# Kernel optimization log

Hardware: AMD Instinct MI355X
Metric: run time of the kernel (lower is better)

The kernel has to match this reference:

```python
import jax, jax.numpy as jnp
from jax import lax
import numpy as np

L, QD, B = 16, 2048, 4096


def setup_inputs() -> dict:
    key = jax.random.key(0)
    k1, k2, k3, k4 = jax.random.split(key, 4)
    input_state = jax.random.normal(k1, (B, QD), dtype=jnp.float32)
    # rotation_angles ~ U(-0.1, 0.1) per _initialize_parameters
    rotation_angles = jax.random.uniform(k2, (L, QD, 3), dtype=jnp.float32, minval=-0.1, maxval=0.1)
    # xavier_uniform for [qd, qd] weights: bound = sqrt(6 / (qd + qd))
    bound = float(np.sqrt(6.0 / (QD + QD)))
    entanglement_weights = jax.random.uniform(k3, (L, QD, QD), dtype=jnp.float32, minval=-bound, maxval=bound)
    # orthogonal init for measurement basis via QR
    m = jax.random.normal(k4, (QD, QD), dtype=jnp.float32)
    q, r = jnp.linalg.qr(m)
    measurement_basis = (q * jnp.sign(jnp.diagonal(r))).astype(jnp.float32)
    return {
        "input_state": input_state,
        "rotation_angles": rotation_angles,
        "entanglement_weights": entanglement_weights,
        "measurement_basis": measurement_basis,
    }


def reference(input_state, rotation_angles, entanglement_weights, measurement_basis):
    # Each rotation gate reduces to an elementwise scale by cos(angle/2):
    #   x-gate: real(rot[0,0]) = cos(a/2); y-gate: cos(a/2); z-gate: real(exp(-i a/2)) = cos(a/2).
    # Fuse all three gates per layer into one per-dim scale: [L, QD]
    scales = jnp.prod(jnp.cos(rotation_angles * 0.5), axis=-1)

    def layer_step(state, layer_params):
        scale, w = layer_params  # scale: [QD], w: [QD, QD]
        return jnp.matmul(state * scale, w), None

    state, _ = lax.scan(layer_step, input_state, (scales, entanglement_weights))
    return jnp.matmul(state, measurement_basis)
```

## Files before the change

kernel.cpp:

```cpp
#include <hip/hip_runtime.h>
#include <stdint.h>

#define L_LAYERS 16
#define QD 2048
#define BATCH 4096

typedef __attribute__((ext_vector_type(8))) __bf16 bf16x8;
typedef __attribute__((ext_vector_type(4))) float f32x4;
typedef __attribute__((address_space(3))) uint32_t lds32_t;
typedef const __attribute__((address_space(1))) uint32_t glob32_t;

__device__ __forceinline__ void async_load16(const void* g, void* l) {
    __builtin_amdgcn_global_load_lds((glob32_t*)(uintptr_t)g, (lds32_t*)(uintptr_t)l,
                                     16, 0, 0);
}

__device__ __forceinline__ unsigned short f2bf(float f) {
    uint32_t u = __float_as_uint(f);
    u += 0x7FFFu + ((u >> 16) & 1u);
    return (unsigned short)(u >> 16);
}

__device__ __forceinline__ float layer_scale(const float* __restrict__ ang,
                                             int lay, int k) {
    const float* ap = ang + ((size_t)lay * QD + k) * 3;
    return __cosf(ap[0] * 0.5f) * __cosf(ap[1] * 0.5f) * __cosf(ap[2] * 0.5f);
}

__global__ void convert_in_kernel(const float* __restrict__ in,
                                  unsigned short* __restrict__ out, int n4) {
    int i = blockIdx.x * 256 + threadIdx.x;
    if (i < n4) {
        float4 v = ((const float4*)in)[i];
        ushort4 o;
        o.x = f2bf(v.x); o.y = f2bf(v.y); o.z = f2bf(v.z); o.w = f2bf(v.w);
        ((ushort4*)out)[i] = o;
    }
}

__global__ void convert_a_all(const float* __restrict__ W, const float* __restrict__ ang,
                              unsigned short* __restrict__ out) {
    const int z = blockIdx.z;
    const float* src = W + (size_t)(2 * z) * QD * QD;
    unsigned short* dst = out + (size_t)z * QD * QD;
    int i = blockIdx.x * 256 + threadIdx.x;
    float s = layer_scale(ang, 2 * z, i >> 9);
    float4 v = ((const float4*)src)[i];
    ushort4 o;
    o.x = f2bf(v.x * s); o.y = f2bf(v.y * s); o.z = f2bf(v.z * s); o.w = f2bf(v.w * s);
    ((ushort4*)dst)[i] = o;
}

__device__ __forceinline__ void conv_tile_body(const float* __restrict__ src,
                                               const float* __restrict__ ang,
                                               int lay,
                                               unsigned short* __restrict__ dst) {
    __shared__ __align__(16) unsigned short tile[64][64];
    const int t = threadIdx.x;
    const int k0 = blockIdx.y * 64, n0 = blockIdx.x * 64;
    const int r = t >> 4;
    const int c = (t & 15) * 4;
    const int g = (t & 7) << 3;
#pragma unroll
    for (int rr = 0; rr < 64; rr += 16) {
        int k = k0 + r + rr;
        float s = (lay >= 0) ? layer_scale(ang, lay, k) : 1.0f;
        float4 v = *(const float4*)(src + (size_t)k * QD + n0 + c);
        int col = (r + rr) ^ g;
        tile[c + 0][col] = f2bf(v.x * s);
        tile[c + 1][col] = f2bf(v.y * s);
        tile[c + 2][col] = f2bf(v.z * s);
        tile[c + 3][col] = f2bf(v.w * s);
    }
    __syncthreads();
    const int wr = t >> 3;
    const int wc = (t & 7) * 8;
#pragma unroll
    for (int rr = 0; rr < 64; rr += 32) {
        int row = wr + rr;
        int pc = wc ^ (((row >> 2) & 7) << 3);
        *(float4*)(dst + (size_t)(n0 + row) * QD + k0 + wc) =
            *(const float4*)(&tile[row][pc]);
    }
}

__global__ void convert_b_all(const float* __restrict__ W, const float* __restrict__ Mb,
                              const float* __restrict__ ang, unsigned short* __restrict__ out) {
    const int z = blockIdx.z;
    const float* src = (z < 8) ? (W + (size_t)(2 * z + 1) * QD * QD) : Mb;
    const int lay = (z < 8) ? (2 * z + 1) : -1;
    unsigned short* dst = out + (size_t)z * QD * QD;
    conv_tile_body(src, ang, lay, dst);
}

struct GemmBatch {
    const unsigned short* a[8];
    const unsigned short* b[8];
    void* c[8];
};

template <int OUT_BF16, int TM>
__global__ __launch_bounds__(256, TM == 128 ? 2 : 4)
void gemm_kernel(GemmBatch args) {
    constexpr int NI = TM / 32;
    __shared__ __align__(16) unsigned short ldsA[TM * 64];
    __shared__ __align__(16) unsigned short ldsB[128 * 64];
    const unsigned short* __restrict__ A  = args.a[blockIdx.z];
    const unsigned short* __restrict__ Bt = args.b[blockIdx.z];
    void* __restrict__ Cout = args.c[blockIdx.z];

    const int t = threadIdx.x;
    const int n0 = blockIdx.x * 128;
    const int m0 = blockIdx.y * TM;
    const int lane = t & 63;
    const int wave = t >> 6;
    const int wm = (wave & 1) * (TM / 2);
    const int wn = (wave >> 1) * 64;
    const int fr = lane & 15;
    const int quad = lane >> 4;

    f32x4 acc[NI][4] = {};

    const int sr = t >> 2;
    const int scol = (t & 3) * 8;
    const unsigned short* ga = A + (size_t)(m0 + sr) * QD + scol;
    const unsigned short* gb = Bt + (size_t)(n0 + sr) * QD + scol;
    unsigned short* la = ldsA + t * 8;
    unsigned short* lb = ldsB + t * 8;

    for (int k0 = 0; k0 < QD; k0 += 64) {
        __syncthreads();
        if constexpr (TM == 128) {
            async_load16(ga, la);
            async_load16(ga + 64 * QD, la + 2048);
            async_load16(ga + 32, la + 4096);
            async_load16(ga + 32 + 64 * QD, la + 6144);
        } else {
            async_load16(ga, la);
            async_load16(ga + 32, la + 2048);
        }
        async_load16(gb, lb);
        async_load16(gb + 64 * QD, lb + 2048);
        async_load16(gb + 32, lb + 4096);
        async_load16(gb + 32 + 64 * QD, lb + 6144);
        ga += 64;
        gb += 64;
        __syncthreads();

#pragma unroll
        for (int kk = 0; kk < 2; kk++) {
            const unsigned short* pa = ldsA + kk * (TM * 32);
            const unsigned short* pb = ldsB + kk * 4096;
            bf16x8 af[NI], bfr[4];
#pragma unroll
            for (int i = 0; i < NI; i++)
                af[i] = *(const bf16x8*)(pa + (wm + i * 16 + fr) * 32 + quad * 8);
#pragma unroll
            for (int j = 0; j < 4; j++)
                bfr[j] = *(const bf16x8*)(pb + (wn + j * 16 + fr) * 32 + quad * 8);
#pragma unroll
            for (int i = 0; i < NI; i++)
#pragma unroll
                for (int j = 0; j < 4; j++)
                    acc[i][j] = __builtin_amdgcn_mfma_f32_16x16x32_bf16(af[i], bfr[j],
                                                                        acc[i][j], 0, 0, 0);
        }
    }

#pragma unroll
    for (int i = 0; i < NI; i++) {
        const int gr = m0 + wm + i * 16 + quad * 4;
#pragma unroll
        for (int j = 0; j < 4; j++) {
            const int gc = n0 + wn + j * 16 + fr;
#pragma unroll
            for (int r = 0; r < 4; r++) {
                float v = acc[i][j][r];
                if (OUT_BF16)
                    ((unsigned short*)Cout)[(size_t)(gr + r) * QD + gc] = f2bf(v);
                else
                    ((float*)Cout)[(size_t)(gr + r) * QD + gc] = v;
            }
        }
    }
}

__device__ __forceinline__ void stage_half(const unsigned short* __restrict__ G,
                                           int row0, int k0,
                                           unsigned char* dst, int t) {
    const int r = t >> 3;
    const int c = 8 * ((t & 7) ^ (r & 7));
    const unsigned short* g = G + (size_t)(row0 + r) * QD + k0 + c;
    async_load16(g, dst + t * 16);
    async_load16(g + 64 * QD, dst + 8192 + t * 16);
}

template <int OUT_BF16>
__global__ __launch_bounds__(512, 2)
void gemm256_kernel(GemmBatch args) {
    __shared__ __align__(16) unsigned char lds[131072];

    const int lin = blockIdx.x + ((blockIdx.y + (blockIdx.z << 3)) << 3);
    const int cpx = gridDim.z << 3;
    const int m = (lin & 7) * cpx + (lin >> 3);
    const int bx = m & 7, by = (m >> 3) & 7, bz = m >> 6;

    const unsigned short* __restrict__ A  = args.a[bz];
    const unsigned short* __restrict__ Bt = args.b[bz];
    void* __restrict__ Cout = args.c[bz];

    const int t = threadIdx.x;
    const int lane = t & 63;
    const int wid = t >> 6;
    const int wm = (wid >> 2) * 128;
    const int wn = (wid & 3) * 64;
    const int fr = lane & 15;
    const int quad = lane >> 4;
    const int m0 = by * 256;
    const int n0 = bx * 256;

    unsigned char* ldsA8 = lds;
    unsigned char* ldsB8 = lds + 65536;
    const int swz45 = (fr & 3) << 4;
    const int frb2 = (fr >> 2) & 1;
    const int kof0 = frb2 << 6;
    const int kof1 = (frb2 ^ 1) << 6;
    const unsigned char* sA = ldsA8 + (wm >> 7) * 16384 + fr * 128 + ((quad * 16) ^ swz45);
    const unsigned char* sB = ldsB8 + ((wn >> 7) & 1) * 16384 + (wn & 64) * 128
                              + fr * 128 + ((quad * 16) ^ swz45);

    f32x4 acc[8][4] = {};
    bf16x8 af[4][2], bfA[2][2], bfB[2][2];

    constexpr int NT = QD / 64;

    stage_half(A,  m0,       0,  ldsA8,         t);
    stage_half(A,  m0 + 128, 0,  ldsA8 + 16384, t);
    stage_half(Bt, n0,       0,  ldsB8,         t);
    stage_half(Bt, n0 + 128, 0,  ldsB8 + 16384, t);
    stage_half(A,  m0,       64, ldsA8 + 32768, t);
    stage_half(Bt, n0,       64, ldsB8 + 32768, t);
    asm volatile("s_waitcnt vmcnt(4)" ::: "memory");
    __builtin_amdgcn_s_barrier();

    for (int kt = 0; kt < NT; ++kt) {
        const int buf  = (kt & 1) << 15;
        const int nbuf = (~kt & 1) << 15;
        const int k1 = ((kt + 1) & (NT - 1)) << 6;
        const int k2 = ((kt + 2) & (NT - 1)) << 6;

#pragma unroll
        for (int mf = 0; mf < 4; mf++)
#pragma unroll
            for (int kk = 0; kk < 2; kk++)
                af[mf][kk] = *(const bf16x8*)(sA + buf + mf * 2048 + (kk ? kof1 : kof0));
#pragma unroll
        for (int nf = 0; nf < 2; nf++)
#pragma unroll
            for (int kk = 0; kk < 2; kk++)
                bfA[nf][kk] = *(const bf16x8*)(sB + buf + nf * 2048 + (kk ? kof1 : kof0));
        stage_half(A, m0 + 128, k1, ldsA8 + nbuf + 16384, t);
        __builtin_amdgcn_s_barrier();
        __builtin_amdgcn_s_setprio(1);
#pragma unroll
        for (int mf = 0; mf < 4; mf++)
#pragma unroll
            for (int nf = 0; nf < 2; nf++)
#pragma unroll
                for (int kk = 0; kk < 2; kk++)
                    acc[mf][nf] = __builtin_amdgcn_mfma_f32_16x16x32_bf16(
                        af[mf][kk], bfA[nf][kk], acc[mf][nf], 0, 0, 0);
        __builtin_amdgcn_s_setprio(0);
        __builtin_amdgcn_s_barrier();

#pragma unroll
        for (int nf = 0; nf < 2; nf++)
#pragma unroll
            for (int kk = 0; kk < 2; kk++)
                bfB[nf][kk] = *(const bf16x8*)(sB + buf + (nf + 2) * 2048 + (kk ? kof1 : kof0));
        stage_half(Bt, n0 + 128, k1, ldsB8 + nbuf + 16384, t);
        __builtin_amdgcn_s_barrier();
        __builtin_amdgcn_s_setprio(1);
#pragma unroll
        for (int mf = 0; mf < 4; mf++)
#pragma unroll
            for (int nf = 0; nf < 2; nf++)
#pragma unroll
                for (int kk = 0; kk < 2; kk++)
                    acc[mf][nf + 2] = __builtin_amdgcn_mfma_f32_16x16x32_bf16(
                        af[mf][kk], bfB[nf][kk], acc[mf][nf + 2], 0, 0, 0);
        __builtin_amdgcn_s_setprio(0);
        __builtin_amdgcn_s_barrier();

#pragma unroll
        for (int mf = 0; mf < 4; mf++)
#pragma unroll
            for (int kk = 0; kk < 2; kk++)
                af[mf][kk] = *(const bf16x8*)(sA + buf + (mf + 4) * 2048 + (kk ? kof1 : kof0));
        stage_half(Bt, n0, k2, ldsB8 + buf, t);
        __builtin_amdgcn_s_barrier();
        __builtin_amdgcn_s_setprio(1);
#pragma unroll
        for (int mf = 0; mf < 4; mf++)
#pragma unroll
            for (int nf = 0; nf < 2; nf++)
#pragma unroll
                for (int kk = 0; kk < 2; kk++)
                    acc[mf + 4][nf + 2] = __builtin_amdgcn_mfma_f32_16x16x32_bf16(
                        af[mf][kk], bfB[nf][kk], acc[mf + 4][nf + 2], 0, 0, 0);
        __builtin_amdgcn_s_setprio(0);
        __builtin_amdgcn_s_barrier();

        stage_half(A, m0, k2, ldsA8 + buf, t);
        __builtin_amdgcn_s_barrier();
        __builtin_amdgcn_s_setprio(1);
#pragma unroll
        for (int mf = 0; mf < 4; mf++)
#pragma unroll
            for (int nf = 0; nf < 2; nf++)
#pragma unroll
                for (int kk = 0; kk < 2; kk++)
                    acc[mf + 4][nf] = __builtin_amdgcn_mfma_f32_16x16x32_bf16(
                        af[mf][kk], bfA[nf][kk], acc[mf + 4][nf], 0, 0, 0);
        __builtin_amdgcn_s_setprio(0);
        asm volatile("s_waitcnt vmcnt(4)" ::: "memory");
        __builtin_amdgcn_s_barrier();
    }

    asm volatile("s_waitcnt vmcnt(0)" ::: "memory");

#pragma unroll
    for (int mf = 0; mf < 8; mf++) {
        const int gr = m0 + wm + mf * 16 + quad * 4;
#pragma unroll
        for (int nf = 0; nf < 4; nf++) {
            const int gc = n0 + wn + nf * 16 + fr;
#pragma unroll
            for (int r = 0; r < 4; r++) {
                float v = acc[mf][nf][r];
                if (OUT_BF16)
                    ((unsigned short*)Cout)[(size_t)(gr + r) * QD + gc] = f2bf(v);
                else
                    ((float*)Cout)[(size_t)(gr + r) * QD + gc] = v;
            }
        }
    }
}

extern "C" void kernel_launch(void* const* d_in, const int* in_sizes, int n_in,
                              void* d_out, int out_size, void* d_ws, size_t ws_size,
                              hipStream_t stream) {
    const float* input_state = (const float*)d_in[0];
    const float* angles      = (const float*)d_in[1];
    const float* W           = (const float*)d_in[2];
    const float* Mb          = (const float*)d_in[3];

    const size_t mat = (size_t)QD * QD;
    char* ws = (char*)d_ws;
    size_t off = 131072;
    unsigned short* xb = (unsigned short*)(ws + off); off += (size_t)BATCH * QD * 2;
    unsigned short* WA = (unsigned short*)(ws + off); off += 8 * mat * 2;
    unsigned short* WB = (unsigned short*)(ws + off); off += 9 * mat * 2;
    unsigned short* T1 = (unsigned short*)(ws + off); off += 8 * mat * 2;
    unsigned short* T2 = (unsigned short*)(ws + off); off += 4 * mat * 2;
    unsigned short* T3 = (unsigned short*)(ws + off); off += 2 * mat * 2;
    unsigned short* T4 = (unsigned short*)(ws + off); off += mat * 2;
    unsigned short* T5 = (unsigned short*)(ws + off); off += mat * 2;

    convert_in_kernel<<<(BATCH * QD / 4) / 256, 256, 0, stream>>>(input_state, xb,
                                                                  BATCH * QD / 4);
    convert_a_all<<<dim3(mat / 4 / 256, 1, 8), 256, 0, stream>>>(W, angles, WA);
    convert_b_all<<<dim3(QD / 64, QD / 64, 9), 256, 0, stream>>>(W, Mb, angles, WB);

    GemmBatch b1{};
    for (int i = 0; i < 8; i++) {
        const unsigned short* wa = WA + (size_t)i * mat;
        const unsigned short* wb = WB + (size_t)i * mat;
        if ((i & 1) == 0) { b1.a[i] = wa; b1.b[i] = wb; }
        else              { b1.a[i] = wb; b1.b[i] = wa; }
        b1.c[i] = T1 + (size_t)i * mat;
    }
    gemm256_kernel<1><<<dim3(QD / 256, QD / 256, 8), 512, 0, stream>>>(b1);

    GemmBatch b2{};
    for (int i = 0; i < 4; i++) {
        b2.a[i] = T1 + (size_t)(2 * i + (i & 1)) * mat;
        b2.b[i] = T1 + (size_t)(2 * i + 1 - (i & 1)) * mat;
        b2.c[i] = T2 + (size_t)i * mat;
    }
    gemm256_kernel<1><<<dim3(QD / 256, QD / 256, 4), 512, 0, stream>>>(b2);

    GemmBatch b3{};
    for (int i = 0; i < 2; i++) {
        b3.a[i] = T2 + (size_t)(2 * i + (i & 1)) * mat;
        b3.b[i] = T2 + (size_t)(2 * i + 1 - (i & 1)) * mat;
        b3.c[i] = T3 + (size_t)i * mat;
    }
    gemm_kernel<1, 128><<<dim3(QD / 128, QD / 128, 2), 256, 0, stream>>>(b3);

    GemmBatch b4{};
    b4.a[0] = T3; b4.b[0] = T3 + mat; b4.c[0] = T4;
    gemm_kernel<1, 64><<<dim3(QD / 128, QD / 64, 1), 256, 0, stream>>>(b4);

    GemmBatch b5{};
    b5.a[0] = WB + 8 * mat; b5.b[0] = T4; b5.c[0] = T5;
    gemm_kernel<1, 64><<<dim3(QD / 128, QD / 64, 1), 256, 0, stream>>>(b5);

    GemmBatch ba{};
    ba.a[0] = xb; ba.b[0] = T5; ba.c[0] = d_out;
    gemm_kernel<0, 128><<<dim3(QD / 128, BATCH / 128, 1), 256, 0, stream>>>(ba);
}
```

Baseline: 733.3 us.

## Split-K the two single-matrix chain GEMMs into halves with fp32 reduction

The two single-matrix 2048^3 GEMMs (T4 and T5) launched only 512 blocks. They are now split along K into two halves that run as a batch of 2, writing fp32 partials, and a separate reduce kernel sums the partials and converts them to bf16. The goal is to double the block count so the GPU's compute units stay better occupied during these sequential stages. In exchange it adds two extra kernel launches and about 32MB of extra fp32 partial traffic per GEMM.

```diff
diff --git a/kernel.cpp b/kernel.cpp
--- a/kernel.cpp
+++ b/kernel.cpp
@@ -93,13 +93,26 @@
     conv_tile_body(src, ang, lay, dst);
 }
 
+__global__ void reduce2_kernel(const float* __restrict__ p0, const float* __restrict__ p1,
+                               unsigned short* __restrict__ dst, int n4) {
+    int i = blockIdx.x * 256 + threadIdx.x;
+    if (i < n4) {
+        float4 a = ((const float4*)p0)[i];
+        float4 b = ((const float4*)p1)[i];
+        ushort4 o;
+        o.x = f2bf(a.x + b.x); o.y = f2bf(a.y + b.y);
+        o.z = f2bf(a.z + b.z); o.w = f2bf(a.w + b.w);
+        ((ushort4*)dst)[i] = o;
+    }
+}
+
 struct GemmBatch {
     const unsigned short* a[8];
     const unsigned short* b[8];
     void* c[8];
 };
 
-template <int OUT_BF16, int TM>
+template <int OUT_BF16, int TM, int KLEN>
 __global__ __launch_bounds__(256, TM == 128 ? 2 : 4)
 void gemm_kernel(GemmBatch args) {
     constexpr int NI = TM / 32;
@@ -128,7 +141,7 @@
     unsigned short* la = ldsA + t * 8;
     unsigned short* lb = ldsB + t * 8;
 
-    for (int k0 = 0; k0 < QD; k0 += 64) {
+    for (int k0 = 0; k0 < KLEN; k0 += 64) {
         __syncthreads();
         if constexpr (TM == 128) {
             async_load16(ga, la);
@@ -366,6 +379,8 @@
     unsigned short* T3 = (unsigned short*)(ws + off); off += 2 * mat * 2;
     unsigned short* T4 = (unsigned short*)(ws + off); off += mat * 2;
     unsigned short* T5 = (unsigned short*)(ws + off); off += mat * 2;
+    float* P0 = (float*)(ws + off); off += mat * 4;
+    float* P1 = (float*)(ws + off); off += mat * 4;
 
     convert_in_kernel<<<(BATCH * QD / 4) / 256, 256, 0, stream>>>(input_state, xb,
                                                                   BATCH * QD / 4);
@@ -396,17 +411,21 @@
         b3.b[i] = T2 + (size_t)(2 * i + 1 - (i & 1)) * mat;
         b3.c[i] = T3 + (size_t)i * mat;
     }
-    gemm_kernel<1, 128><<<dim3(QD / 128, QD / 128, 2), 256, 0, stream>>>(b3);
+    gemm_kernel<1, 128, QD><<<dim3(QD / 128, QD / 128, 2), 256, 0, stream>>>(b3);
 
     GemmBatch b4{};
-    b4.a[0] = T3; b4.b[0] = T3 + mat; b4.c[0] = T4;
-    gemm_kernel<1, 64><<<dim3(QD / 128, QD / 64, 1), 256, 0, stream>>>(b4);
+    b4.a[0] = T3;        b4.b[0] = T3 + mat;        b4.c[0] = P0;
+    b4.a[1] = T3 + 1024; b4.b[1] = T3 + mat + 1024; b4.c[1] = P1;
+    gemm_kernel<0, 64, 1024><<<dim3(QD / 128, QD / 64, 2), 256, 0, stream>>>(b4);
+    reduce2_kernel<<<(mat / 4 + 255) / 256, 256, 0, stream>>>(P0, P1, T4, mat / 4);
 
     GemmBatch b5{};
-    b5.a[0] = WB + 8 * mat; b5.b[0] = T4; b5.c[0] = T5;
-    gemm_kernel<1, 64><<<dim3(QD / 128, QD / 64, 1), 256, 0, stream>>>(b5);
+    b5.a[0] = WB + 8 * mat;        b5.b[0] = T4;        b5.c[0] = P0;
+    b5.a[1] = WB + 8 * mat + 1024; b5.b[1] = T4 + 1024; b5.c[1] = P1;
+    gemm_kernel<0, 64, 1024><<<dim3(QD / 128, QD / 64, 2), 256, 0, stream>>>(b5);
+    reduce2_kernel<<<(mat / 4 + 255) / 256, 256, 0, stream>>>(P0, P1, T5, mat / 4);
 
     GemmBatch ba{};
     ba.a[0] = xb; ba.b[0] = T5; ba.c[0] = d_out;
-    gemm_kernel<0, 128><<<dim3(QD / 128, BATCH / 128, 1), 256, 0, stream>>>(ba);
-}
+    gemm_kernel<0, 128, QD><<<dim3(QD / 128, BATCH / 128, 1), 256, 0, stream>>>(ba);
+}
```

New measurement: 744.6 us. About the same (+1.5%).
